# Optimization experiments

Measured on AMD Instinct MI355X. Metric: run time of the kernel, lower is better.

## Reference

```python
import jax, jax.numpy as jnp
import numpy as np

B, S, C = 8, 2048, 1024
DROPOUT_RATE = 0.1


def setup_inputs() -> dict:
    key = jax.random.key(0)
    k1, k2, k3 = jax.random.split(key, 3)
    x = jax.random.normal(k1, (B, S, C), dtype=jnp.float32)
    # Fixed orthogonal projection buffer, as in __init__: U from SVD of a random matrix
    rand_mat = jax.random.normal(k2, (C, C), dtype=jnp.float32)
    U, _, _ = jnp.linalg.svd(rand_mat)
    U = U.astype(jnp.float32)
    # Base random permutation of [0, C)
    perm = jax.random.permutation(k3, C).astype(jnp.int32)
    # Stand-in for random.randint(0, 1000), fixed for determinism
    randint = 123
    return {"x": x, "U": U, "perm": perm, "randint": randint}


def reference(x, U, perm, randint):
    # channel_dim == -1, so the transpose in the original forward is a no-op.
    rand_scale = (DROPOUT_RATE / (1.0 - DROPOUT_RATE)) ** 0.5
    n = x.shape[-1]
    b = x.size // n
    # _randperm_like: per-row permutation ans[b_, i] = perm[i] * (6*randint*b_ + 1) mod n.
    # Reduce the multiplier mod n first so int32 arithmetic never overflows
    # (math is identical since (a*b) % n == (a*(b%n)) % n).
    batch_rand = (jnp.arange(b, dtype=jnp.int32) * (randint * 6) + 1) % n  # [b]
    ans = (perm[None, :] * batch_rand[:, None]) % n                        # [b, n]
    ans = ans.reshape(x.shape)                                             # same shape as x

    x_g = jnp.take_along_axis(x, ans, axis=-1)   # gather per-row permuted channels
    y = jnp.matmul(x_g, U)                        # shared (C,C) projection
    # scatter_(-1, ans, y) places y[..., j] at position ans[..., j]; since ans is a
    # permutation per row, this equals gathering y with the inverse permutation.
    inv = jnp.argsort(ans, axis=-1)
    x_next = jnp.take_along_axis(y, inv, axis=-1)
    return x_next * rand_scale + x
```

## Files before the change

### kernel.cpp

```cpp
#include <hip/hip_runtime.h>
#include <hip/hip_bf16.h>

#define WS_UT    ((size_t)0)
#define WS_XG    ((size_t)2*1024*1024)

typedef __attribute__((ext_vector_type(8))) short short8;
typedef __attribute__((ext_vector_type(4))) float floatx4;

__device__ __forceinline__ void load_lds16(const void* g, void* l) {
  __builtin_amdgcn_global_load_lds(
      (const __attribute__((address_space(1))) void*)g,
      (__attribute__((address_space(3))) void*)l, 16, 0, 0);
}

__device__ __forceinline__ unsigned short f2bf(float f) {
  __hip_bfloat16 h = __float2bfloat16(f);
  return __builtin_bit_cast(unsigned short, h);
}
__device__ __forceinline__ float bf2f(unsigned short u) {
  return __uint_as_float(((unsigned)u) << 16);
}

__global__ void __launch_bounds__(256) prep_gather_k(const float* __restrict__ U,
                                                     const float* __restrict__ x,
                                                     const int* __restrict__ perm,
                                                     const int* __restrict__ prand,
                                                     unsigned short* __restrict__ ut,
                                                     unsigned short* __restrict__ xg) {
  __shared__ __align__(16) char smem[64 * 65 * 4];
  if (blockIdx.x < 256) {
    float (*tile)[65] = (float (*)[65])smem;
    const int tn = (blockIdx.x & 15) * 64;
    const int tk = (blockIdx.x >> 4) * 64;
    const int r = threadIdx.x >> 6;
    const int c = threadIdx.x & 63;
    for (int s = 0; s < 16; ++s)
      tile[s * 4 + r][c] = U[(size_t)(tk + s * 4 + r) * 1024 + tn + c];
    __syncthreads();
    for (int s = 0; s < 16; ++s)
      ut[(size_t)(tn + s * 4 + r) * 1024 + tk + c] = f2bf(tile[c][s * 4 + r]);
    return;
  }
  float (*xrow)[1024] = (float (*)[1024])smem;
  const int w = threadIdx.x >> 6, lane = threadIdx.x & 63;
  const int row = (blockIdx.x - 256) * 4 + w;
  const unsigned mult = ((unsigned)prand[0] * 6u) & 1023u;
  const unsigned br = (((unsigned)row & 1023u) * mult + 1u) & 1023u;
  const float* xr = x + (size_t)row * 1024;
  unsigned short* xo = xg + (size_t)row * 1024;
  for (int t = 0; t < 4; ++t) {
    floatx4 v = *(const floatx4*)(xr + t * 256 + lane * 4);
    *(floatx4*)(&xrow[w][t * 256 + lane * 4]) = v;
  }
  __syncthreads();
  for (int t = 0; t < 4; ++t) {
    int i0 = t * 256 + lane * 4;
    int4 p = *(const int4*)(perm + i0);
    ushort4 o;
    o.x = f2bf(xrow[w][((unsigned)p.x * br) & 1023u]);
    o.y = f2bf(xrow[w][((unsigned)p.y * br) & 1023u]);
    o.z = f2bf(xrow[w][((unsigned)p.z * br) & 1023u]);
    o.w = f2bf(xrow[w][((unsigned)p.w * br) & 1023u]);
    *(ushort4*)(xo + i0) = o;
  }
}

__global__ void __launch_bounds__(512, 1) gemm_scatter_k(
    const unsigned short* __restrict__ xg,
    const unsigned short* __restrict__ ut,
    const int* __restrict__ perm,
    const int* __restrict__ prand,
    float* __restrict__ out) {
  __shared__ __align__(16) char smem[65536];
  const int tid = threadIdx.x;
  const int w = tid >> 6, lane = tid & 63;
  const int m = lane & 15, q = lane >> 4;
  const int R0 = blockIdx.x * 64;
  const int wn = w * 128;

  const int x3 = m & 7;
  const int qq = q ^ (x3 & 3);
  const int sf = x3 >> 2;
  const int offA0 = m * 128 + (qq + sf * 4) * 16;
  const int offA1 = m * 128 + (qq + 4 - sf * 4) * 16;

  const int sr = lane >> 3, sslot = lane & 7;
  const unsigned short* asrc =
      xg + (size_t)(R0 + w * 8 + sr) * 1024 + (size_t)((sslot ^ sr) * 8);
  char* adst0 = smem + w * 1024 + lane * 16;

  const unsigned short* bb[8];
#pragma unroll
  for (int jj = 0; jj < 8; ++jj)
    bb[jj] = ut + (size_t)(wn + jj * 16 + m) * 1024 + q * 8;

  floatx4 acc[4][8];
#pragma unroll
  for (int i = 0; i < 4; ++i)
#pragma unroll
    for (int jj = 0; jj < 8; ++jj) acc[i][jj] = (floatx4)0.0f;

  load_lds16(asrc, adst0);
  __syncthreads();

#pragma unroll
  for (int kt = 0; kt < 16; ++kt) {
    const char* Ac = smem + (kt & 1) * 8192;
    short8 b0[8];
#pragma unroll
    for (int jj = 0; jj < 8; ++jj)
      b0[jj] = *(const short8*)(bb[jj] + kt * 64);
    if (kt < 15)
      load_lds16(asrc + (kt + 1) * 64, adst0 + ((kt + 1) & 1) * 8192);
    short8 a0[4];
#pragma unroll
    for (int i = 0; i < 4; ++i) a0[i] = *(const short8*)(Ac + i * 2048 + offA0);
    short8 b1[8];
#pragma unroll
    for (int jj = 0; jj < 8; ++jj)
      b1[jj] = *(const short8*)(bb[jj] + kt * 64 + 32);
#pragma unroll
    for (int i = 0; i < 4; ++i)
#pragma unroll
      for (int jj = 0; jj < 8; ++jj)
        acc[i][jj] = __builtin_amdgcn_mfma_f32_16x16x32_bf16(b0[jj], a0[i],
                                                             acc[i][jj], 0, 0, 0);
    short8 a1[4];
#pragma unroll
    for (int i = 0; i < 4; ++i) a1[i] = *(const short8*)(Ac + i * 2048 + offA1);
#pragma unroll
    for (int i = 0; i < 4; ++i)
#pragma unroll
      for (int jj = 0; jj < 8; ++jj)
        acc[i][jj] = __builtin_amdgcn_mfma_f32_16x16x32_bf16(b1[jj], a1[i],
                                                             acc[i][jj], 0, 0, 0);
    __syncthreads();
  }

  const unsigned mult = ((unsigned)prand[0] * 6u) & 1023u;
  const float rs = 0.33333334f;
  float* sbuf = (float*)smem;
#pragma unroll
  for (int i = 0; i < 4; ++i) {
    const int row = R0 + i * 16 + m;
    const unsigned br = (((unsigned)row & 1023u) * mult + 1u) & 1023u;
    const unsigned short* xr = xg + (size_t)row * 1024;
#pragma unroll
    for (int jj = 0; jj < 8; ++jj) {
      const int j0 = wn + jj * 16 + q * 4;
      const int4 p4 = *(const int4*)(perm + j0);
      const ushort4 x4 = *(const ushort4*)(xr + j0);
      sbuf[m * 1024 + (((unsigned)p4.x * br) & 1023u)] = rs * acc[i][jj][0] + bf2f(x4.x);
      sbuf[m * 1024 + (((unsigned)p4.y * br) & 1023u)] = rs * acc[i][jj][1] + bf2f(x4.y);
      sbuf[m * 1024 + (((unsigned)p4.z * br) & 1023u)] = rs * acc[i][jj][2] + bf2f(x4.z);
      sbuf[m * 1024 + (((unsigned)p4.w * br) & 1023u)] = rs * acc[i][jj][3] + bf2f(x4.w);
    }
    __syncthreads();
    float* orow0 = out + (size_t)(R0 + i * 16) * 1024;
#pragma unroll
    for (int v = 0; v < 8; ++v) {
      const int f = v * 512 + tid;
      *(floatx4*)(orow0 + ((f >> 8) * 1024 + (f & 255) * 4)) =
          *(const floatx4*)(sbuf + (size_t)f * 4);
    }
    if (i < 3) __syncthreads();
  }
}

extern "C" void kernel_launch(void* const* d_in, const int* in_sizes, int n_in,
                              void* d_out, int out_size, void* d_ws, size_t ws_size,
                              hipStream_t stream) {
  const float* x = (const float*)d_in[0];
  const float* U = (const float*)d_in[1];
  const int* perm = (const int*)d_in[2];
  const int* prand = (const int*)d_in[3];
  float* out = (float*)d_out;
  char* ws = (char*)d_ws;
  unsigned short* ut = (unsigned short*)(ws + WS_UT);
  unsigned short* xg = (unsigned short*)(ws + WS_XG);

  prep_gather_k<<<256 + 4096, 256, 0, stream>>>(U, x, perm, prand, ut, xg);
  gemm_scatter_k<<<256, 512, 0, stream>>>(xg, ut, perm, prand, out);
}
```

Baseline: 200.7 us.

## Stage B operand tiles through LDS instead of direct global register loads

The GEMM kernel now copies both the A (gathered x) tile and a full 1024x64 slice of the transposed U into LDS each k-step via global_load_lds, and reads B fragments from LDS with the same swizzle as A. This replaces per-lane strided global loads of B, which had poor coalescing, and uses 136 KB of dynamic shared memory. In exchange the A double-buffering is removed: loads and compute are serialized around a barrier per k-step, and the loop is no longer unrolled. The epilogue scatter buffer now fits in the larger dynamic LDS.

```diff
diff --git a/kernel.cpp b/kernel.cpp
--- a/kernel.cpp
+++ b/kernel.cpp
@@ -71,7 +71,9 @@
     const int* __restrict__ perm,
     const int* __restrict__ prand,
     float* __restrict__ out) {
-  __shared__ __align__(16) char smem[65536];
+  extern __shared__ __align__(16) char smem[];
+  char* Abuf = smem;
+  char* Bbuf = smem + 8192;
   const int tid = threadIdx.x;
   const int w = tid >> 6, lane = tid & 63;
   const int m = lane & 15, q = lane >> 4;
@@ -81,18 +83,16 @@
   const int x3 = m & 7;
   const int qq = q ^ (x3 & 3);
   const int sf = x3 >> 2;
-  const int offA0 = m * 128 + (qq + sf * 4) * 16;
-  const int offA1 = m * 128 + (qq + 4 - sf * 4) * 16;
+  const int offF0 = m * 128 + (qq + sf * 4) * 16;
+  const int offF1 = m * 128 + (qq + 4 - sf * 4) * 16;
 
   const int sr = lane >> 3, sslot = lane & 7;
   const unsigned short* asrc =
       xg + (size_t)(R0 + w * 8 + sr) * 1024 + (size_t)((sslot ^ sr) * 8);
-  char* adst0 = smem + w * 1024 + lane * 16;
-
-  const unsigned short* bb[8];
-#pragma unroll
-  for (int jj = 0; jj < 8; ++jj)
-    bb[jj] = ut + (size_t)(wn + jj * 16 + m) * 1024 + q * 8;
+  char* adst = Abuf + w * 1024 + lane * 16;
+  const unsigned short* bsrc =
+      ut + (size_t)(w * 128 + sr) * 1024 + (size_t)((sslot ^ sr) * 8);
+  char* bdst = Bbuf + w * 16384 + lane * 16;
 
   floatx4 acc[4][8];
 #pragma unroll
@@ -100,34 +100,32 @@
 #pragma unroll
     for (int jj = 0; jj < 8; ++jj) acc[i][jj] = (floatx4)0.0f;
 
-  load_lds16(asrc, adst0);
-  __syncthreads();
-
+#pragma unroll 1
+  for (int kt = 0; kt < 16; ++kt) {
+    const int k0 = kt * 64;
+    load_lds16(asrc + k0, adst);
 #pragma unroll
-  for (int kt = 0; kt < 16; ++kt) {
-    const char* Ac = smem + (kt & 1) * 8192;
-    short8 b0[8];
+    for (int t = 0; t < 16; ++t)
+      load_lds16(bsrc + (size_t)t * 8192 + k0, bdst + t * 1024);
+    __syncthreads();
+    short8 a0[4], b0[8];
+#pragma unroll
+    for (int i = 0; i < 4; ++i) a0[i] = *(const short8*)(Abuf + i * 2048 + offF0);
 #pragma unroll
     for (int jj = 0; jj < 8; ++jj)
-      b0[jj] = *(const short8*)(bb[jj] + kt * 64);
-    if (kt < 15)
-      load_lds16(asrc + (kt + 1) * 64, adst0 + ((kt + 1) & 1) * 8192);
-    short8 a0[4];
-#pragma unroll
-    for (int i = 0; i < 4; ++i) a0[i] = *(const short8*)(Ac + i * 2048 + offA0);
-    short8 b1[8];
-#pragma unroll
-    for (int jj = 0; jj < 8; ++jj)
-      b1[jj] = *(const short8*)(bb[jj] + kt * 64 + 32);
+      b0[jj] = *(const short8*)(Bbuf + wn * 128 + jj * 2048 + offF0);
 #pragma unroll
     for (int i = 0; i < 4; ++i)
 #pragma unroll
       for (int jj = 0; jj < 8; ++jj)
         acc[i][jj] = __builtin_amdgcn_mfma_f32_16x16x32_bf16(b0[jj], a0[i],
                                                              acc[i][jj], 0, 0, 0);
-    short8 a1[4];
+    short8 a1[4], b1[8];
 #pragma unroll
-    for (int i = 0; i < 4; ++i) a1[i] = *(const short8*)(Ac + i * 2048 + offA1);
+    for (int i = 0; i < 4; ++i) a1[i] = *(const short8*)(Abuf + i * 2048 + offF1);
+#pragma unroll
+    for (int jj = 0; jj < 8; ++jj)
+      b1[jj] = *(const short8*)(Bbuf + wn * 128 + jj * 2048 + offF1);
 #pragma unroll
     for (int i = 0; i < 4; ++i)
 #pragma unroll
@@ -179,6 +177,9 @@
   unsigned short* ut = (unsigned short*)(ws + WS_UT);
   unsigned short* xg = (unsigned short*)(ws + WS_XG);
 
+  hipFuncSetAttribute((const void*)gemm_scatter_k,
+                      hipFuncAttributeMaxDynamicSharedMemorySize, 139264);
+
   prep_gather_k<<<256 + 4096, 256, 0, stream>>>(U, x, perm, prand, ut, xg);
-  gemm_scatter_k<<<256, 512, 0, stream>>>(xg, ut, perm, prand, out);
+  gemm_scatter_k<<<256, 512, 139264, stream>>>(xg, ut, perm, prand, out);
 }
```

Result: faster. 172.0 us (-14.3%).

## Drop LDS staging of A in GEMM and use 16 waves reading operands directly

Applied to the files above, without the earlier changes.

The GEMM kernel no longer stages the gathered activation tile in LDS through async global_load_lds double buffering. Each wave now loads both A and B fragments straight from global memory and relies on the caches for reuse. The block grows from 512 to 1024 threads, so each wave covers 64 output columns instead of 128 with a smaller accumulator set. This removes the per-k-step barriers and LDS traffic, but it gives up explicit A reuse and adds global/L2 load pressure.

```diff
diff --git a/kernel.cpp b/kernel.cpp
--- a/kernel.cpp
+++ b/kernel.cpp
@@ -6,12 +6,6 @@
 
 typedef __attribute__((ext_vector_type(8))) short short8;
 typedef __attribute__((ext_vector_type(4))) float floatx4;
-
-__device__ __forceinline__ void load_lds16(const void* g, void* l) {
-  __builtin_amdgcn_global_load_lds(
-      (const __attribute__((address_space(1))) void*)g,
-      (__attribute__((address_space(3))) void*)l, 16, 0, 0);
-}
 
 __device__ __forceinline__ unsigned short f2bf(float f) {
   __hip_bfloat16 h = __float2bfloat16(f);
@@ -65,88 +59,64 @@
   }
 }
 
-__global__ void __launch_bounds__(512, 1) gemm_scatter_k(
+__global__ void __launch_bounds__(1024) gemm_scatter_k(
     const unsigned short* __restrict__ xg,
     const unsigned short* __restrict__ ut,
     const int* __restrict__ perm,
     const int* __restrict__ prand,
     float* __restrict__ out) {
-  __shared__ __align__(16) char smem[65536];
+  __shared__ __align__(16) float sbuf[16 * 1024];
   const int tid = threadIdx.x;
   const int w = tid >> 6, lane = tid & 63;
   const int m = lane & 15, q = lane >> 4;
   const int R0 = blockIdx.x * 64;
-  const int wn = w * 128;
+  const int wn = w * 64;
 
-  const int x3 = m & 7;
-  const int qq = q ^ (x3 & 3);
-  const int sf = x3 >> 2;
-  const int offA0 = m * 128 + (qq + sf * 4) * 16;
-  const int offA1 = m * 128 + (qq + 4 - sf * 4) * 16;
+  const unsigned short* ua[4];
+  const unsigned short* ub[4];
+#pragma unroll
+  for (int i = 0; i < 4; ++i) ua[i] = xg + (size_t)(R0 + i * 16) * 1024;
+#pragma unroll
+  for (int jj = 0; jj < 4; ++jj) ub[jj] = ut + (size_t)jj * 16 * 1024;
+  const int va = m * 1024 + q * 8;
+  const int vb = (wn + m) * 1024 + q * 8;
 
-  const int sr = lane >> 3, sslot = lane & 7;
-  const unsigned short* asrc =
-      xg + (size_t)(R0 + w * 8 + sr) * 1024 + (size_t)((sslot ^ sr) * 8);
-  char* adst0 = smem + w * 1024 + lane * 16;
-
-  const unsigned short* bb[8];
-#pragma unroll
-  for (int jj = 0; jj < 8; ++jj)
-    bb[jj] = ut + (size_t)(wn + jj * 16 + m) * 1024 + q * 8;
-
-  floatx4 acc[4][8];
+  floatx4 acc[4][4];
 #pragma unroll
   for (int i = 0; i < 4; ++i)
 #pragma unroll
-    for (int jj = 0; jj < 8; ++jj) acc[i][jj] = (floatx4)0.0f;
-
-  load_lds16(asrc, adst0);
-  __syncthreads();
+    for (int jj = 0; jj < 4; ++jj) acc[i][jj] = (floatx4)0.0f;
 
 #pragma unroll
   for (int kt = 0; kt < 16; ++kt) {
-    const char* Ac = smem + (kt & 1) * 8192;
-    short8 b0[8];
 #pragma unroll
-    for (int jj = 0; jj < 8; ++jj)
-      b0[jj] = *(const short8*)(bb[jj] + kt * 64);
-    if (kt < 15)
-      load_lds16(asrc + (kt + 1) * 64, adst0 + ((kt + 1) & 1) * 8192);
-    short8 a0[4];
+    for (int s = 0; s < 2; ++s) {
+      const int kp = kt * 64 + s * 32;
+      short8 b[4], a[4];
 #pragma unroll
-    for (int i = 0; i < 4; ++i) a0[i] = *(const short8*)(Ac + i * 2048 + offA0);
-    short8 b1[8];
+      for (int jj = 0; jj < 4; ++jj)
+        b[jj] = *(const short8*)(ub[jj] + vb + kp);
 #pragma unroll
-    for (int jj = 0; jj < 8; ++jj)
-      b1[jj] = *(const short8*)(bb[jj] + kt * 64 + 32);
+      for (int i = 0; i < 4; ++i)
+        a[i] = *(const short8*)(ua[i] + va + kp);
 #pragma unroll
-    for (int i = 0; i < 4; ++i)
+      for (int i = 0; i < 4; ++i)
 #pragma unroll
-      for (int jj = 0; jj < 8; ++jj)
-        acc[i][jj] = __builtin_amdgcn_mfma_f32_16x16x32_bf16(b0[jj], a0[i],
-                                                             acc[i][jj], 0, 0, 0);
-    short8 a1[4];
-#pragma unroll
-    for (int i = 0; i < 4; ++i) a1[i] = *(const short8*)(Ac + i * 2048 + offA1);
-#pragma unroll
-    for (int i = 0; i < 4; ++i)
-#pragma unroll
-      for (int jj = 0; jj < 8; ++jj)
-        acc[i][jj] = __builtin_amdgcn_mfma_f32_16x16x32_bf16(b1[jj], a1[i],
-                                                             acc[i][jj], 0, 0, 0);
-    __syncthreads();
+        for (int jj = 0; jj < 4; ++jj)
+          acc[i][jj] = __builtin_amdgcn_mfma_f32_16x16x32_bf16(b[jj], a[i],
+                                                               acc[i][jj], 0, 0, 0);
+    }
   }
 
   const unsigned mult = ((unsigned)prand[0] * 6u) & 1023u;
   const float rs = 0.33333334f;
-  float* sbuf = (float*)smem;
 #pragma unroll
   for (int i = 0; i < 4; ++i) {
     const int row = R0 + i * 16 + m;
     const unsigned br = (((unsigned)row & 1023u) * mult + 1u) & 1023u;
     const unsigned short* xr = xg + (size_t)row * 1024;
 #pragma unroll
-    for (int jj = 0; jj < 8; ++jj) {
+    for (int jj = 0; jj < 4; ++jj) {
       const int j0 = wn + jj * 16 + q * 4;
       const int4 p4 = *(const int4*)(perm + j0);
       const ushort4 x4 = *(const ushort4*)(xr + j0);
@@ -158,8 +128,8 @@
     __syncthreads();
     float* orow0 = out + (size_t)(R0 + i * 16) * 1024;
 #pragma unroll
-    for (int v = 0; v < 8; ++v) {
-      const int f = v * 512 + tid;
+    for (int v = 0; v < 4; ++v) {
+      const int f = v * 1024 + tid;
       *(floatx4*)(orow0 + ((f >> 8) * 1024 + (f & 255) * 4)) =
           *(const floatx4*)(sbuf + (size_t)f * 4);
     }
@@ -180,5 +150,5 @@
   unsigned short* xg = (unsigned short*)(ws + WS_XG);
 
   prep_gather_k<<<256 + 4096, 256, 0, stream>>>(U, x, perm, prand, ut, xg);
-  gemm_scatter_k<<<256, 512, 0, stream>>>(xg, ut, perm, prand, out);
+  gemm_scatter_k<<<256, 1024, 0, stream>>>(xg, ut, perm, prand, out);
 }
```

Measured after the change: 244.1 us. 1.22x slower.
